# Performance work log

Hardware: AMD Instinct MI355X
Metric: run time of the kernel (lower is better)

Reference implementation:

```python
import jax, jax.numpy as jnp
import numpy as np

B, H, N, D = 8, 12, 1024, 64
SCALE = 1.0 / float(np.sqrt(D))  # 0.125; torch forward default is 1.0 but 1/sqrt(d) is the production value
EPS = 1e-06


def setup_inputs() -> dict:
    key = jax.random.key(0)
    kq, kk, kv = jax.random.split(key, 3)
    q = jax.random.normal(kq, (B, H, N, D), dtype=jnp.float32)
    k = jax.random.normal(kk, (B, H, N, D), dtype=jnp.float32)
    v = jax.random.normal(kv, (B, H, N, D), dtype=jnp.float32)
    # Parameter init per L2Q.__init__: alpha=0.125, beta=0.5, gamma=1/n_tokens
    alpha = jnp.full((H, 1, 1), 0.125, dtype=jnp.float32)
    beta = jnp.full((H, 1, 1), 0.5, dtype=jnp.float32)
    gamma = jnp.full((H, 1, 1), 1.0 / N, dtype=jnp.float32)
    return {"q": q, "k": k, "v": v, "alpha": alpha, "beta": beta, "gamma": gamma}


def reference(q, k, v, alpha, beta, gamma):
    # logits: (B, H, N, N)
    logits = jnp.einsum("bhnd,bhmd->bhnm", q, k) * SCALE
    # per-head quadratic polynomial, then ReLU; params (H,1,1) broadcast over (B,H,N,N)
    attn = jax.nn.relu(alpha * logits * logits + beta * logits + gamma)
    attn = attn / (jnp.sum(attn, axis=-1, keepdims=True) + EPS)
    return jnp.einsum("bhnm,bhmd->bhnd", attn, v)
```

## Files before the change

### kernel.cpp

```cpp
#include <hip/hip_runtime.h>
#include <hip/hip_bf16.h>

typedef __attribute__((ext_vector_type(8))) short bf16x8;
typedef __attribute__((ext_vector_type(4))) float f32x4;
typedef __attribute__((ext_vector_type(16))) float f32x16;

#define MFMA16(a, b, c) __builtin_amdgcn_mfma_f32_16x16x32_bf16(a, b, c, 0, 0, 0)
#define MFMA32(a, b, c) __builtin_amdgcn_mfma_f32_32x32x16_bf16(a, b, c, 0, 0, 0)

static constexpr int kH = 12;
static constexpr int kN = 1024;
static constexpr int kD = 64;
static constexpr int kBH = 96;
static constexpr int kND = kN * kD;
static constexpr float kScale = 0.125f;
static constexpr float kEps = 1e-6f;
static constexpr long kTensorElems = (long)kBH * kND;
static constexpr long kWsNeeded = 2 * kTensorElems * 2;

__device__ __forceinline__ unsigned bfbits(float x) {
    union { __hip_bfloat16 h; unsigned short u; } c;
    c.h = __float2bfloat16(x);
    return (unsigned)c.u;
}
__device__ __forceinline__ unsigned pack2_rne(float a, float b) {
    return bfbits(a) | (bfbits(b) << 16);
}
__device__ __forceinline__ unsigned pack2_rhu(float lo, float hi) {
    unsigned a = __builtin_bit_cast(unsigned, lo) + 0x8000u;
    unsigned b = __builtin_bit_cast(unsigned, hi) + 0x8000u;
    return __builtin_amdgcn_perm(b, a, 0x07060302u);
}
__device__ __forceinline__ void gl_lds16(const void* g, void* l) {
    __builtin_amdgcn_global_load_lds(
        (const __attribute__((address_space(1))) void*)g,
        (__attribute__((address_space(3))) void*)l, 16, 0, 0);
}

__global__ __launch_bounds__(256, 2) void prep(
    const float* __restrict__ k, const float* __restrict__ v,
    unsigned* __restrict__ kbf, unsigned* __restrict__ vtb)
{
    static constexpr int TS = 68;
    __shared__ float T32[64 * TS];
    const int bid = blockIdx.x;
    const int bh = bid >> 4, nt = bid & 15;
    const int t = threadIdx.x;

    const float* kp = k + (long)bh * kND + (long)nt * 64 * kD;
    unsigned* ko = kbf + ((long)bh * kND + (long)nt * 64 * kD) / 2;
#pragma unroll
    for (int r = 0; r < 4; ++r) {
        const int f4 = t + 256 * r;
        const float4 f = ((const float4*)kp)[f4];
        uint2 u;
        u.x = pack2_rne(f.x, f.y);
        u.y = pack2_rne(f.z, f.w);
        *(uint2*)&ko[f4 * 2] = u;
    }

    const float* vp = v + (long)bh * kND + (long)nt * 64 * kD;
#pragma unroll
    for (int r = 0; r < 4; ++r) {
        const int f4 = t + 256 * r;
        const int n = f4 >> 4, d4 = f4 & 15;
        const float4 f = *(const float4*)(vp + (long)n * kD + 4 * d4);
        *(float4*)&T32[n * TS + 4 * d4] = f;
    }
    __syncthreads();
    const int d = t >> 2, c = t & 3;
    unsigned u[8];
#pragma unroll
    for (int j = 0; j < 8; ++j) {
        const int key = c * 16 + 2 * j;
        u[j] = pack2_rne(T32[key * TS + d], T32[(key + 1) * TS + d]);
    }
    uint4 A, B;
    A.x = u[0]; A.y = u[1]; A.z = u[4]; A.w = u[5];
    B.x = u[2]; B.y = u[3]; B.z = u[6]; B.w = u[7];
    unsigned* vbase = vtb + (long)bh * (kND / 2);
    const long o0 = (long)nt * 2048 + ((d >> 5) * 4 + c) * 256 + (d & 31) * 4;
    *(uint4*)(vbase + o0)       = A;
    *(uint4*)(vbase + o0 + 128) = B;
}

__global__ __launch_bounds__(256, 3) void l2q_main(
    const float* __restrict__ q,
    const unsigned short* __restrict__ kbf, const unsigned short* __restrict__ vtbf,
    const float* __restrict__ alpha, const float* __restrict__ beta, const float* __restrict__ gamma,
    float* __restrict__ out)
{
    __shared__ __align__(16) unsigned Ks[2][2048];

    const int bid  = blockIdx.x;
    const int xcd  = bid & 7;
    const int sIdx = bid >> 3;
    const int bh   = xcd * 12 + (sIdx % 12);
    const int qt   = sIdx / 12;
    const int h    = bh % kH;
    const int t    = threadIdx.x;
    const int wave = t >> 6;
    const int lane = t & 63;
    const int l31  = lane & 31;
    const int hh   = lane >> 5;

    const float al = alpha[h] * (kScale * kScale);
    const float be = beta[h] * kScale;
    const float ga = gamma[h];

    const float* qp = q + (long)bh * kND;
    const unsigned short* kp = kbf + (long)bh * kND;
    const unsigned* vlin = (const unsigned*)vtbf + (long)bh * (kND / 2);

    bf16x8 qbF[4];
    {
        const int qrow = qt * 128 + wave * 32 + l31;
        const float* qsrc = qp + (long)qrow * kD;
#pragma unroll
        for (int s = 0; s < 4; ++s) {
            const float4 f0 = *(const float4*)(qsrc + s * 16 + hh * 8);
            const float4 f1 = *(const float4*)(qsrc + s * 16 + hh * 8 + 4);
            uint4 u;
            u.x = pack2_rne(f0.x, f0.y);
            u.y = pack2_rne(f0.z, f0.w);
            u.z = pack2_rne(f1.x, f1.y);
            u.w = pack2_rne(f1.z, f1.w);
            qbF[s] = __builtin_bit_cast(bf16x8, u);
        }
    }

    f32x16 oacc[2];
#pragma unroll
    for (int db = 0; db < 2; ++db)
#pragma unroll
        for (int r = 0; r < 16; ++r)
            oacc[db][r] = 0.f;
    float dacc[4] = {0.f, 0.f, 0.f, 0.f};

    const int srow8 = lane >> 3;
    const int g8    = lane & 7;
    auto stageK = [&](int buf, int tile) {
        const int k0 = tile * 64;
#pragma unroll
        for (int c = 0; c < 2; ++c) {
            const int seg = c * 4 + wave;
            const int r = seg * 8 + srow8;
            gl_lds16(kp + (long)(k0 + r) * kD + (g8 ^ srow8) * 8, &Ks[buf][seg * 256]);
        }
    };

    stageK(0, 0);

    for (int tile = 0; tile < 16; ++tile) {
        const int buf = tile & 1;
        __syncthreads();
        if (tile + 1 < 16) stageK(buf ^ 1, tile + 1);

        const unsigned* vt0 = vlin + (long)tile * 2048 + (hh * 32 + l31) * 4;
        bf16x8 vfr[2][4];
#pragma unroll
        for (int db = 0; db < 2; ++db)
#pragma unroll
            for (int s = 0; s < 4; ++s)
                vfr[db][s] = *(const bf16x8*)(vt0 + (db * 4 + s) * 256);

        const unsigned* Kb = Ks[buf];

        f32x16 st[2];
#pragma unroll
        for (int kb = 0; kb < 2; ++kb)
#pragma unroll
            for (int r = 0; r < 16; ++r)
                st[kb][r] = 0.f;
#pragma unroll
        for (int s = 0; s < 4; ++s) {
            const int g = (s << 1) | hh;
#pragma unroll
            for (int kb = 0; kb < 2; ++kb) {
                const int row = kb * 32 + l31;
                bf16x8 ka = *(const bf16x8*)&Kb[row * 32 + ((g ^ (row & 7)) << 2)];
                st[kb] = MFMA32(ka, qbF[s], st[kb]);
            }
        }

        unsigned u[2][8];
#pragma unroll
        for (int kb = 0; kb < 2; ++kb) {
#pragma unroll
            for (int p = 0; p < 8; ++p) {
                const float s0 = st[kb][2 * p], s1 = st[kb][2 * p + 1];
                const float w0 = fmaxf(fmaf(fmaf(al, s0, be), s0, ga), 0.f);
                const float w1 = fmaxf(fmaf(fmaf(al, s1, be), s1, ga), 0.f);
                dacc[p & 3] += w0 + w1;
                u[kb][p] = pack2_rhu(w0, w1);
            }
        }

#pragma unroll
        for (int s = 0; s < 4; ++s) {
            uint4 fr;
            const int kb = s >> 1, b = (s & 1) * 4;
            fr.x = u[kb][b + 0];
            fr.y = u[kb][b + 1];
            fr.z = u[kb][b + 2];
            fr.w = u[kb][b + 3];
            const bf16x8 pa = __builtin_bit_cast(bf16x8, fr);
            oacc[0] = MFMA32(pa, vfr[0][s], oacc[0]);
            oacc[1] = MFMA32(pa, vfr[1][s], oacc[1]);
        }
    }

    float d = (dacc[0] + dacc[1]) + (dacc[2] + dacc[3]);
    d += __shfl_xor(d, 32);
    const float inv = 1.0f / (d + kEps);

    const long obase = (long)bh * kND;
    const int rowbase = qt * 128 + wave * 32;
#pragma unroll
    for (int r = 0; r < 16; ++r) {
        const int row32 = (r & 3) + 8 * (r >> 2) + 4 * hh;
        const float iv = __shfl(inv, row32);
        float* o = out + obase + (long)(rowbase + row32) * kD + l31;
        o[0]  = oacc[0][r] * iv;
        o[32] = oacc[1][r] * iv;
    }
}

static constexpr int KSU = 36;
static constexpr int VSU = 36;
static constexpr int PSU = 36;

__global__ __launch_bounds__(256, 3) void l2q_attn_fb(
    const float* __restrict__ q, const float* __restrict__ k, const float* __restrict__ v,
    const float* __restrict__ alpha, const float* __restrict__ beta, const float* __restrict__ gamma,
    float* __restrict__ out)
{
    __shared__ __align__(16) unsigned KsU[64 * KSU];
    __shared__ __align__(16) unsigned VtU[64 * VSU];
    __shared__ __align__(16) unsigned PU[128 * PSU];

    const int bid  = blockIdx.x;
    const int bh   = bid >> 3;
    const int qt   = bid & 7;
    const int h    = bh % kH;
    const int t    = threadIdx.x;
    const int wave = t >> 6;
    const int lane = t & 63;
    const int quad = lane >> 4;
    const int l15  = lane & 15;

    const float al = alpha[h], be = beta[h], ga = gamma[h];

    const long base = (long)bh * kN * kD;
    const float* qp = q + base;
    const float* kp = k + base;
    const float* vp = v + base;

    bf16x8 qa[2][2];
#pragma unroll
    for (int rb = 0; rb < 2; ++rb) {
        const int row = qt * 128 + wave * 32 + rb * 16 + l15;
#pragma unroll
        for (int kc = 0; kc < 2; ++kc) {
            const float* src = qp + (long)row * kD + kc * 32 + quad * 8;
            const float4 f0 = *(const float4*)(src);
            const float4 f1 = *(const float4*)(src + 4);
            uint4 u;
            u.x = pack2_rne(f0.x, f0.y);
            u.y = pack2_rne(f0.z, f0.w);
            u.z = pack2_rne(f1.x, f1.y);
            u.w = pack2_rne(f1.z, f1.w);
            qa[rb][kc] = __builtin_bit_cast(bf16x8, u);
        }
    }

    f32x4 oacc[2][4];
#pragma unroll
    for (int rb = 0; rb < 2; ++rb)
#pragma unroll
        for (int db = 0; db < 4; ++db)
            oacc[rb][db] = (f32x4){0.f, 0.f, 0.f, 0.f};

    float dsum[2][4] = {{0.f, 0.f, 0.f, 0.f}, {0.f, 0.f, 0.f, 0.f}};
    unsigned* Pw = &PU[wave * 32 * PSU];

    for (int tile = 0; tile < 16; ++tile) {
        __syncthreads();
        const int k0 = tile * 64;
#pragma unroll
        for (int r = 0; r < 4; ++r) {
            const int f4 = t + 256 * r;
            const int n = f4 >> 4, d4 = f4 & 15;
            const float4 kg = *(const float4*)(kp + (long)(k0 + n) * kD + 4 * d4);
            uint2 pk;
            pk.x = pack2_rne(kg.x, kg.y);
            pk.y = pack2_rne(kg.z, kg.w);
            *(uint2*)&KsU[n * KSU + 2 * d4] = pk;
        }
#pragma unroll
        for (int r = 0; r < 2; ++r) {
            const int u = t + 256 * r;
            const int key2 = u & 31, d4 = u >> 5;
            const float* s0 = vp + (long)(k0 + 2 * key2) * kD + 4 * d4;
            const float4 va = *(const float4*)(s0);
            const float4 vb = *(const float4*)(s0 + kD);
            VtU[(4 * d4 + 0) * VSU + key2] = pack2_rne(va.x, vb.x);
            VtU[(4 * d4 + 1) * VSU + key2] = pack2_rne(va.y, vb.y);
            VtU[(4 * d4 + 2) * VSU + key2] = pack2_rne(va.z, vb.z);
            VtU[(4 * d4 + 3) * VSU + key2] = pack2_rne(va.w, vb.w);
        }
        __syncthreads();

        f32x4 s[2][4];
#pragma unroll
        for (int rb = 0; rb < 2; ++rb)
#pragma unroll
            for (int nb = 0; nb < 4; ++nb)
                s[rb][nb] = (f32x4){0.f, 0.f, 0.f, 0.f};
#pragma unroll
        for (int nb = 0; nb < 4; ++nb) {
            bf16x8 kb0 = *(const bf16x8*)&KsU[(nb * 16 + l15) * KSU + 4 * quad];
            bf16x8 kb1 = *(const bf16x8*)&KsU[(nb * 16 + l15) * KSU + 16 + 4 * quad];
#pragma unroll
            for (int rb = 0; rb < 2; ++rb) {
                s[rb][nb] = MFMA16(qa[rb][0], kb0, s[rb][nb]);
                s[rb][nb] = MFMA16(qa[rb][1], kb1, s[rb][nb]);
            }
        }

        const bool ev = (lane & 1) == 0;
#pragma unroll
        for (int rb = 0; rb < 2; ++rb) {
#pragma unroll
            for (int nb = 0; nb < 4; ++nb) {
                float w0, w1, w2, w3;
                {
                    float l0 = s[rb][nb][0] * kScale;
                    float l1 = s[rb][nb][1] * kScale;
                    float l2 = s[rb][nb][2] * kScale;
                    float l3 = s[rb][nb][3] * kScale;
                    w0 = fmaxf(fmaf(fmaf(al, l0, be), l0, ga), 0.f);
                    w1 = fmaxf(fmaf(fmaf(al, l1, be), l1, ga), 0.f);
                    w2 = fmaxf(fmaf(fmaf(al, l2, be), l2, ga), 0.f);
                    w3 = fmaxf(fmaf(fmaf(al, l3, be), l3, ga), 0.f);
                }
                dsum[rb][0] += w0; dsum[rb][1] += w1;
                dsum[rb][2] += w2; dsum[rb][3] += w3;

                const float o0 = __shfl_xor(w0, 1);
                const float o1 = __shfl_xor(w1, 1);
                const float o2 = __shfl_xor(w2, 1);
                const float o3 = __shfl_xor(w3, 1);
                const unsigned pa = ev ? pack2_rne(w0, o0) : pack2_rne(o2, w2);
                const unsigned pb = ev ? pack2_rne(w1, o1) : pack2_rne(o3, w3);
                const int r0 = ev ? 0 : 2;
                const int cu = (16 * nb + (l15 & ~1)) >> 1;
                const int rowb = rb * 16 + quad * 4 + r0;
                Pw[rowb * PSU + cu] = pa;
                Pw[(rowb + 1) * PSU + cu] = pb;
            }
        }

        bf16x8 pf[2][2];
#pragma unroll
        for (int rb = 0; rb < 2; ++rb)
#pragma unroll
            for (int kc = 0; kc < 2; ++kc)
                pf[rb][kc] = *(const bf16x8*)&Pw[(rb * 16 + l15) * PSU + 16 * kc + 4 * quad];
#pragma unroll
        for (int db = 0; db < 4; ++db) {
            bf16x8 vf0 = *(const bf16x8*)&VtU[(db * 16 + l15) * VSU + 4 * quad];
            bf16x8 vf1 = *(const bf16x8*)&VtU[(db * 16 + l15) * VSU + 16 + 4 * quad];
#pragma unroll
            for (int rb = 0; rb < 2; ++rb) {
                oacc[rb][db] = MFMA16(pf[rb][0], vf0, oacc[rb][db]);
                oacc[rb][db] = MFMA16(pf[rb][1], vf1, oacc[rb][db]);
            }
        }
    }

#pragma unroll
    for (int rb = 0; rb < 2; ++rb)
#pragma unroll
        for (int i = 0; i < 4; ++i) {
            float d = dsum[rb][i];
            d += __shfl_xor(d, 1);
            d += __shfl_xor(d, 2);
            d += __shfl_xor(d, 4);
            d += __shfl_xor(d, 8);
            dsum[rb][i] = 1.0f / (d + kEps);
        }

#pragma unroll
    for (int rb = 0; rb < 2; ++rb)
#pragma unroll
        for (int db = 0; db < 4; ++db)
#pragma unroll
            for (int i = 0; i < 4; ++i) {
                const int row = qt * 128 + wave * 32 + rb * 16 + quad * 4 + i;
                out[base + (long)row * kD + db * 16 + l15] = oacc[rb][db][i] * dsum[rb][i];
            }
}

extern "C" void kernel_launch(void* const* d_in, const int* in_sizes, int n_in,
                              void* d_out, int out_size, void* d_ws, size_t ws_size,
                              hipStream_t stream) {
    const float* q     = (const float*)d_in[0];
    const float* k     = (const float*)d_in[1];
    const float* v     = (const float*)d_in[2];
    const float* alpha = (const float*)d_in[3];
    const float* beta  = (const float*)d_in[4];
    const float* gamma = (const float*)d_in[5];
    float* out = (float*)d_out;

    if (ws_size < (size_t)kWsNeeded) {
        l2q_attn_fb<<<dim3(768), dim3(256), 0, stream>>>(q, k, v, alpha, beta, gamma, out);
        return;
    }

    unsigned* kbf = (unsigned*)d_ws;
    unsigned* vtb = kbf + kTensorElems / 2;

    prep<<<dim3(1536), dim3(256), 0, stream>>>(k, v, kbf, vtb);
    l2q_main<<<dim3(768), dim3(256), 0, stream>>>(
        q, (const unsigned short*)kbf, (const unsigned short*)vtb,
        alpha, beta, gamma, out);
}
```

Before: 145.3 us.

## Pre-swizzle K into MFMA fragment layout and load directly from global

The prep kernel now writes K in bf16 already arranged in per-lane MFMA fragment order, the same way V was arranged. The main kernel drops its LDS double-buffered K staging and the per-tile __syncthreads, and each lane loads its K and V fragments straight from global/L2 with 16-byte loads. This removes LDS traffic and barriers in the main loop. In exchange there is no explicit prefetch, so global latency is exposed unless the compiler or occupancy hides it, and prep gains an extra LDS pass.

```diff
diff --git a/kernel.cpp b/kernel.cpp
--- a/kernel.cpp
+++ b/kernel.cpp
@@ -31,15 +31,10 @@
     unsigned b = __builtin_bit_cast(unsigned, hi) + 0x8000u;
     return __builtin_amdgcn_perm(b, a, 0x07060302u);
 }
-__device__ __forceinline__ void gl_lds16(const void* g, void* l) {
-    __builtin_amdgcn_global_load_lds(
-        (const __attribute__((address_space(1))) void*)g,
-        (__attribute__((address_space(3))) void*)l, 16, 0, 0);
-}
 
 __global__ __launch_bounds__(256, 2) void prep(
     const float* __restrict__ k, const float* __restrict__ v,
-    unsigned* __restrict__ kbf, unsigned* __restrict__ vtb)
+    unsigned* __restrict__ klin, unsigned* __restrict__ vlin)
 {
     static constexpr int TS = 68;
     __shared__ float T32[64 * TS];
@@ -48,40 +43,59 @@
     const int t = threadIdx.x;
 
     const float* kp = k + (long)bh * kND + (long)nt * 64 * kD;
-    unsigned* ko = kbf + ((long)bh * kND + (long)nt * 64 * kD) / 2;
-#pragma unroll
-    for (int r = 0; r < 4; ++r) {
-        const int f4 = t + 256 * r;
-        const float4 f = ((const float4*)kp)[f4];
-        uint2 u;
-        u.x = pack2_rne(f.x, f.y);
-        u.y = pack2_rne(f.z, f.w);
-        *(uint2*)&ko[f4 * 2] = u;
-    }
-
-    const float* vp = v + (long)bh * kND + (long)nt * 64 * kD;
 #pragma unroll
     for (int r = 0; r < 4; ++r) {
         const int f4 = t + 256 * r;
         const int n = f4 >> 4, d4 = f4 & 15;
-        const float4 f = *(const float4*)(vp + (long)n * kD + 4 * d4);
-        *(float4*)&T32[n * TS + 4 * d4] = f;
+        *(float4*)&T32[n * TS + 4 * d4] = *(const float4*)(kp + (long)n * kD + 4 * d4);
     }
     __syncthreads();
-    const int d = t >> 2, c = t & 3;
-    unsigned u[8];
-#pragma unroll
-    for (int j = 0; j < 8; ++j) {
-        const int key = c * 16 + 2 * j;
-        u[j] = pack2_rne(T32[key * TS + d], T32[(key + 1) * TS + d]);
-    }
-    uint4 A, B;
-    A.x = u[0]; A.y = u[1]; A.z = u[4]; A.w = u[5];
-    B.x = u[2]; B.y = u[3]; B.z = u[6]; B.w = u[7];
-    unsigned* vbase = vtb + (long)bh * (kND / 2);
-    const long o0 = (long)nt * 2048 + ((d >> 5) * 4 + c) * 256 + (d & 31) * 4;
-    *(uint4*)(vbase + o0)       = A;
-    *(uint4*)(vbase + o0 + 128) = B;
+    {
+        const int f = t >> 5, sub = t & 31;
+        const int s = f >> 1, kb = f & 1;
+        unsigned* kdst = klin + (long)bh * (kND / 2) + (long)nt * 2048 + f * 256 + sub * 8;
+        uint4 o0, o1;
+#pragma unroll
+        for (int e = 0; e < 2; ++e) {
+            const int l = sub * 2 + e;
+            const int hh = l >> 5, l31 = l & 31;
+            const float* srcf = &T32[(kb * 32 + l31) * TS + (s * 2 + hh) * 8];
+            uint4 o;
+            o.x = pack2_rne(srcf[0], srcf[1]);
+            o.y = pack2_rne(srcf[2], srcf[3]);
+            o.z = pack2_rne(srcf[4], srcf[5]);
+            o.w = pack2_rne(srcf[6], srcf[7]);
+            if (e == 0) o0 = o; else o1 = o;
+        }
+        *(uint4*)(kdst)     = o0;
+        *(uint4*)(kdst + 4) = o1;
+    }
+    __syncthreads();
+
+    const float* vp = v + (long)bh * kND + (long)nt * 64 * kD;
+#pragma unroll
+    for (int r = 0; r < 4; ++r) {
+        const int f4 = t + 256 * r;
+        const int n = f4 >> 4, d4 = f4 & 15;
+        *(float4*)&T32[n * TS + 4 * d4] = *(const float4*)(vp + (long)n * kD + 4 * d4);
+    }
+    __syncthreads();
+    {
+        const int d = t >> 2, c = t & 3;
+        unsigned u[8];
+#pragma unroll
+        for (int j = 0; j < 8; ++j) {
+            const int key = c * 16 + 2 * j;
+            u[j] = pack2_rne(T32[key * TS + d], T32[(key + 1) * TS + d]);
+        }
+        uint4 A, B;
+        A.x = u[0]; A.y = u[1]; A.z = u[4]; A.w = u[5];
+        B.x = u[2]; B.y = u[3]; B.z = u[6]; B.w = u[7];
+        unsigned* vbase = vlin + (long)bh * (kND / 2);
+        const long o0 = (long)nt * 2048 + ((d >> 5) * 4 + c) * 256 + (d & 31) * 4;
+        *(uint4*)(vbase + o0)       = A;
+        *(uint4*)(vbase + o0 + 128) = B;
+    }
 }
 
 __global__ __launch_bounds__(256, 3) void l2q_main(
@@ -90,8 +104,6 @@
     const float* __restrict__ alpha, const float* __restrict__ beta, const float* __restrict__ gamma,
     float* __restrict__ out)
 {
-    __shared__ __align__(16) unsigned Ks[2][2048];
-
     const int bid  = blockIdx.x;
     const int xcd  = bid & 7;
     const int sIdx = bid >> 3;
@@ -109,8 +121,9 @@
     const float ga = gamma[h];
 
     const float* qp = q + (long)bh * kND;
-    const unsigned short* kp = kbf + (long)bh * kND;
+    const unsigned* klin = (const unsigned*)kbf + (long)bh * (kND / 2);
     const unsigned* vlin = (const unsigned*)vtbf + (long)bh * (kND / 2);
+    const int lane4 = (hh * 32 + l31) * 4;
 
     bf16x8 qbF[4];
     {
@@ -137,34 +150,17 @@
             oacc[db][r] = 0.f;
     float dacc[4] = {0.f, 0.f, 0.f, 0.f};
 
-    const int srow8 = lane >> 3;
-    const int g8    = lane & 7;
-    auto stageK = [&](int buf, int tile) {
-        const int k0 = tile * 64;
-#pragma unroll
-        for (int c = 0; c < 2; ++c) {
-            const int seg = c * 4 + wave;
-            const int r = seg * 8 + srow8;
-            gl_lds16(kp + (long)(k0 + r) * kD + (g8 ^ srow8) * 8, &Ks[buf][seg * 256]);
-        }
-    };
-
-    stageK(0, 0);
-
     for (int tile = 0; tile < 16; ++tile) {
-        const int buf = tile & 1;
-        __syncthreads();
-        if (tile + 1 < 16) stageK(buf ^ 1, tile + 1);
-
-        const unsigned* vt0 = vlin + (long)tile * 2048 + (hh * 32 + l31) * 4;
-        bf16x8 vfr[2][4];
-#pragma unroll
-        for (int db = 0; db < 2; ++db)
-#pragma unroll
-            for (int s = 0; s < 4; ++s)
-                vfr[db][s] = *(const bf16x8*)(vt0 + (db * 4 + s) * 256);
-
-        const unsigned* Kb = Ks[buf];
+        const unsigned* kt0 = klin + (long)tile * 2048 + lane4;
+        const unsigned* vt0 = vlin + (long)tile * 2048 + lane4;
+        bf16x8 kfr[8];
+        bf16x8 vfr[8];
+#pragma unroll
+        for (int f = 0; f < 8; ++f)
+            kfr[f] = *(const bf16x8*)(kt0 + f * 256);
+#pragma unroll
+        for (int f = 0; f < 8; ++f)
+            vfr[f] = *(const bf16x8*)(vt0 + f * 256);
 
         f32x16 st[2];
 #pragma unroll
@@ -173,15 +169,10 @@
             for (int r = 0; r < 16; ++r)
                 st[kb][r] = 0.f;
 #pragma unroll
-        for (int s = 0; s < 4; ++s) {
-            const int g = (s << 1) | hh;
-#pragma unroll
-            for (int kb = 0; kb < 2; ++kb) {
-                const int row = kb * 32 + l31;
-                bf16x8 ka = *(const bf16x8*)&Kb[row * 32 + ((g ^ (row & 7)) << 2)];
-                st[kb] = MFMA32(ka, qbF[s], st[kb]);
-            }
-        }
+        for (int s = 0; s < 4; ++s)
+#pragma unroll
+            for (int kb = 0; kb < 2; ++kb)
+                st[kb] = MFMA32(kfr[s * 2 + kb], qbF[s], st[kb]);
 
         unsigned u[2][8];
 #pragma unroll
@@ -205,8 +196,8 @@
             fr.z = u[kb][b + 2];
             fr.w = u[kb][b + 3];
             const bf16x8 pa = __builtin_bit_cast(bf16x8, fr);
-            oacc[0] = MFMA32(pa, vfr[0][s], oacc[0]);
-            oacc[1] = MFMA32(pa, vfr[1][s], oacc[1]);
+            oacc[0] = MFMA32(pa, vfr[s], oacc[0]);
+            oacc[1] = MFMA32(pa, vfr[4 + s], oacc[1]);
         }
     }
 
@@ -418,11 +409,11 @@
         return;
     }
 
-    unsigned* kbf = (unsigned*)d_ws;
-    unsigned* vtb = kbf + kTensorElems / 2;
-
-    prep<<<dim3(1536), dim3(256), 0, stream>>>(k, v, kbf, vtb);
+    unsigned* klin = (unsigned*)d_ws;
+    unsigned* vlin = klin + kTensorElems / 2;
+
+    prep<<<dim3(1536), dim3(256), 0, stream>>>(k, v, klin, vlin);
     l2q_main<<<dim3(768), dim3(256), 0, stream>>>(
-        q, (const unsigned short*)kbf, (const unsigned short*)vtb,
+        q, (const unsigned short*)klin, (const unsigned short*)vlin,
         alpha, beta, gamma, out);
 }
```

Result: no change. 146.6 us (+0.9%).
